# Performance work log

Measured on AMD Instinct MI355X. Metric: run time of the kernel, lower is better.

## Reference

```python
import jax, jax.numpy as jnp
import numpy as np

# Blade metric for Cl(1,3) inner product <~A B>_0: sign per basis blade =
# (-1)^{k(k-1)/2} * prod(eta_ii) with eta = diag(1,-1,-1,-1).
# Order: 1 | e0 e1 e2 e3 | e01 e02 e03 e12 e13 e23 | e012 e013 e023 e123 | e0123
BLADE_METRIC = jnp.array(
    [1.0,
     1.0, -1.0, -1.0, -1.0,
     1.0, 1.0, 1.0, -1.0, -1.0, -1.0,
     -1.0, -1.0, -1.0, 1.0,
     -1.0],
    dtype=jnp.float32,
)

B, H, N, MVC, SC = 8, 8, 1024, 8, 32


def setup_inputs() -> dict:
    key = jax.random.key(0)
    ks = jax.random.split(key, 6)
    mv_shape = (B, H, N, MVC, 16)
    s_shape = (B, H, N, SC)
    return {
        "q_mv": jax.random.normal(ks[0], mv_shape, dtype=jnp.float32),
        "k_mv": jax.random.normal(ks[1], mv_shape, dtype=jnp.float32),
        "v_mv": jax.random.normal(ks[2], mv_shape, dtype=jnp.float32),
        "q_s": jax.random.normal(ks[3], s_shape, dtype=jnp.float32),
        "k_s": jax.random.normal(ks[4], s_shape, dtype=jnp.float32),
        "v_s": jax.random.normal(ks[5], s_shape, dtype=jnp.float32),
    }


def reference(q_mv, k_mv, v_mv, q_s, k_s, v_s):
    *lead, n_out, mvc, _ = q_mv.shape
    n_in = k_mv.shape[-3]
    sc = q_s.shape[-1]
    d = 16 * mvc + sc  # total feature dim used for the softmax scale

    # Apply GA blade metric to queries, flatten mv channels, concat scalars.
    qf = jnp.concatenate(
        [(q_mv * BLADE_METRIC).reshape(*lead, n_out, mvc * 16), q_s], axis=-1
    )
    kf = jnp.concatenate([k_mv.reshape(*lead, n_in, mvc * 16), k_s], axis=-1)
    vf = jnp.concatenate([v_mv.reshape(*lead, n_in, mvc * 16), v_s], axis=-1)

    scores = jnp.einsum("bhid,bhjd->bhij", qf, kf) / jnp.sqrt(
        jnp.asarray(d, dtype=qf.dtype)
    )
    attn = jax.nn.softmax(scores, axis=-1)
    out = jnp.einsum("bhij,bhjd->bhid", attn, vf)

    out_mv = out[..., : mvc * 16].reshape(*lead, n_out, mvc, 16)
    out_s = out[..., mvc * 16 :]
    return out_mv, out_s
```

## Files before the change

### kernel.cpp

```cpp
#include <hip/hip_runtime.h>

typedef __attribute__((ext_vector_type(8))) _Float16 f16x8;
typedef __attribute__((ext_vector_type(4))) float f32x4;

#define BHn 64
#define Nn 1024

static constexpr int kOutMvElems = 8 * 8 * 1024 * 128;
static constexpr float kScaleLog2e = 0.11405506f;
static constexpr unsigned kNegMask = 0xBF1Cu;
static constexpr int kBlob = 20480;

typedef __attribute__((address_space(1))) const void* gas1_t;
typedef __attribute__((address_space(3))) void* las3_t;
__device__ __forceinline__ void dma16(const _Float16* g, _Float16* l) {
  __builtin_amdgcn_global_load_lds((gas1_t)g, (las3_t)l, 16, 0, 0);
}

__global__ __launch_bounds__(256) void pack_kernel(const float* __restrict__ kmv,
                                                   const float* __restrict__ ks,
                                                   const float* __restrict__ vmv,
                                                   const float* __restrict__ vs,
                                                   _Float16* __restrict__ KV) {
  __shared__ _Float16 tk[64][184];
  __shared__ _Float16 tv[160][72];
  const int kt = blockIdx.x;
  const int bh = blockIdx.y;
  const int tid = threadIdx.x;
#pragma unroll
  for (int i = 0; i < 5; ++i) {
    int s = tid + 256 * i;
    int key = s / 20, p = s - key * 20;
    int row = bh * Nn + kt * 64 + key;
    const float* src = (p < 16) ? (kmv + (size_t)row * 128 + p * 8)
                                : (ks + (size_t)row * 32 + (p - 16) * 8);
    float4 a = *(const float4*)src;
    float4 b = *(const float4*)(src + 4);
    f16x8 h;
    h[0] = (_Float16)a.x; h[1] = (_Float16)a.y; h[2] = (_Float16)a.z; h[3] = (_Float16)a.w;
    h[4] = (_Float16)b.x; h[5] = (_Float16)b.y; h[6] = (_Float16)b.z; h[7] = (_Float16)b.w;
    *(f16x8*)&tk[key][p * 8] = h;
  }
  for (int s = tid; s < 64 * 40; s += 256) {
    int key = s / 40, p = s - key * 40;
    int row = bh * Nn + kt * 64 + key;
    const float* src = (p < 32) ? (vmv + (size_t)row * 128 + p * 4)
                                : (vs + (size_t)row * 32 + (p - 32) * 4);
    float4 v = *(const float4*)src;
    int d = p * 4;
    tv[d + 0][key] = (_Float16)v.x;
    tv[d + 1][key] = (_Float16)v.y;
    tv[d + 2][key] = (_Float16)v.z;
    tv[d + 3][key] = (_Float16)v.w;
  }
  __syncthreads();
  _Float16* dst = KV + ((size_t)bh * 16 + kt) * kBlob;
#pragma unroll
  for (int i = 0; i < 5; ++i) {
    int u = tid + 256 * i;
    int p = u >> 6, key = u & 63;
    f16x8 h = *(const f16x8*)&tk[key][p * 8];
    *(f16x8*)&dst[p * 512 + key * 8] = h;
  }
#pragma unroll
  for (int i = 0; i < 5; ++i) {
    int u = tid + 256 * i;
    int s = u / 160, d = u - s * 160;
    int c32 = (s >> 2) * 32, gg = s & 3;
    f16x8 h;
#pragma unroll
    for (int i2 = 0; i2 < 8; ++i2) {
      int key = c32 + ((i2 < 4) ? (gg * 4 + i2) : (16 + gg * 4 + (i2 - 4)));
      h[i2] = tv[d][key];
    }
    *(f16x8*)&dst[10240 + u * 8] = h;
  }
}

__global__ __launch_bounds__(512, 2) void geo_attn_kernel(const float* __restrict__ qmv,
                                                          const float* __restrict__ qs,
                                                          const _Float16* __restrict__ KV,
                                                          float* __restrict__ out) {
  __shared__ __align__(16) _Float16 kv[2 * kBlob];

  const int b = blockIdx.x;
  const int sw = (b & 7) * 32 + (b >> 3);
  const int qb = sw & 3;
  const int bh = sw >> 2;

  const int tid = threadIdx.x;
  const int w = tid >> 6;
  const int l = tid & 63;
  const int g = l >> 4;
  const int nn = l & 15;

  const _Float16* blob0 = KV + (size_t)bh * 16 * kBlob;

  int kbase[5];
#pragma unroll
  for (int c = 0; c < 5; ++c) kbase[c] = (4 * c + g) * 512 + nn * 8;
  int vbase[2];
#pragma unroll
  for (int ch = 0; ch < 2; ++ch) vbase[ch] = 10240 + (4 * ch + g) * 1280 + nn * 8;

  f16x8 qf[2][5];
#pragma unroll
  for (int q2 = 0; q2 < 2; ++q2) {
    const size_t qbase = (size_t)(bh * Nn + qb * 256 + w * 32 + q2 * 16 + nn);
#pragma unroll
    for (int c = 0; c < 5; ++c) {
      const float* src = (c < 4) ? (qmv + qbase * 128 + c * 32 + 8 * g)
                                 : (qs + qbase * 32 + 8 * g);
      float4 a = *(const float4*)src;
      float4 bb = *(const float4*)(src + 4);
      float x[8] = {a.x, a.y, a.z, a.w, bb.x, bb.y, bb.z, bb.w};
#pragma unroll
      for (int i = 0; i < 8; ++i) {
        float v = x[i] * kScaleLog2e;
        if (c < 4) {
          int idx = ((g & 1) << 3) + i;
          v = ((kNegMask >> idx) & 1u) ? -v : v;
        }
        qf[q2][c][i] = (_Float16)v;
      }
    }
  }

  f32x4 acc[2][10];
#pragma unroll
  for (int q2 = 0; q2 < 2; ++q2)
#pragma unroll
    for (int j = 0; j < 10; ++j) acc[q2][j] = (f32x4){0.f, 0.f, 0.f, 0.f};
  float Ma = 12.f, Mb = 12.f, La = 0.f, Lb = 0.f;

  f32x4 sa[4], sb[4];
  f16x8 paf[2], pbf[2];

  const int laneOff = l * 8 + w * 512;
  auto stage = [&](int t, int buf) {
    const _Float16* src = blob0 + (size_t)t * kBlob + laneOff;
    _Float16* dst = &kv[buf * kBlob + w * 512];
#pragma unroll
    for (int i = 0; i < 5; ++i) dma16(src + i * 4096, dst + i * 4096);
  };
  auto do_qk = [&](int buf) {
    const _Float16* kb_ = &kv[buf * kBlob];
#pragma unroll
    for (int kb = 0; kb < 4; ++kb) {
      sa[kb] = (f32x4){0.f, 0.f, 0.f, 0.f};
      sb[kb] = (f32x4){0.f, 0.f, 0.f, 0.f};
    }
#pragma unroll
    for (int c = 0; c < 5; ++c) {
      f16x8 kf[4];
#pragma unroll
      for (int kb = 0; kb < 4; ++kb) kf[kb] = *(const f16x8*)&kb_[kbase[c] + kb * 128];
#pragma unroll
      for (int kb = 0; kb < 4; ++kb) {
        sa[kb] = __builtin_amdgcn_mfma_f32_16x16x32_f16(kf[kb], qf[0][c], sa[kb], 0, 0, 0);
        sb[kb] = __builtin_amdgcn_mfma_f32_16x16x32_f16(kf[kb], qf[1][c], sb[kb], 0, 0, 0);
      }
    }
  };
  auto do_pv = [&](int buf) {
    const _Float16* vb_ = &kv[buf * kBlob];
#pragma unroll
    for (int ch = 0; ch < 2; ++ch)
#pragma unroll
      for (int j = 0; j < 10; ++j) {
        f16x8 vb = *(const f16x8*)&vb_[vbase[ch] + j * 128];
        acc[0][j] = __builtin_amdgcn_mfma_f32_16x16x32_f16(paf[ch], vb, acc[0][j], 0, 0, 0);
        acc[1][j] = __builtin_amdgcn_mfma_f32_16x16x32_f16(pbf[ch], vb, acc[1][j], 0, 0, 0);
      }
  };
  auto do_softmax = [&]() {
    float lma = fmaxf(fmaxf(fmaxf(fmaxf(sa[0][0], sa[0][1]), fmaxf(sa[0][2], sa[0][3])),
                            fmaxf(fmaxf(sa[1][0], sa[1][1]), fmaxf(sa[1][2], sa[1][3]))),
                      fmaxf(fmaxf(fmaxf(sa[2][0], sa[2][1]), fmaxf(sa[2][2], sa[2][3])),
                            fmaxf(fmaxf(sa[3][0], sa[3][1]), fmaxf(sa[3][2], sa[3][3]))));
    float lmb = fmaxf(fmaxf(fmaxf(fmaxf(sb[0][0], sb[0][1]), fmaxf(sb[0][2], sb[0][3])),
                            fmaxf(fmaxf(sb[1][0], sb[1][1]), fmaxf(sb[1][2], sb[1][3]))),
                      fmaxf(fmaxf(fmaxf(sb[2][0], sb[2][1]), fmaxf(sb[2][2], sb[2][3])),
                            fmaxf(fmaxf(sb[3][0], sb[3][1]), fmaxf(sb[3][2], sb[3][3]))));
    bool need = (lma - Ma > 8.f) || (lmb - Mb > 8.f);
    if (__any((int)need)) {
      float pma = fmaxf(lma, __shfl_xor(lma, 16));
      pma = fmaxf(pma, __shfl_xor(pma, 32));
      float pmb = fmaxf(lmb, __shfl_xor(lmb, 16));
      pmb = fmaxf(pmb, __shfl_xor(pmb, 32));
      float nMa = fmaxf(Ma, pma); float fsa = exp2f(Ma - nMa); Ma = nMa;
      float nMb = fmaxf(Mb, pmb); float fsb = exp2f(Mb - nMb); Mb = nMb;
      La *= fsa; Lb *= fsb;
      float fa[4], fb[4];
#pragma unroll
      for (int r = 0; r < 4; ++r) {
        fa[r] = __shfl(fsa, 4 * g + r, 16);
        fb[r] = __shfl(fsb, 4 * g + r, 16);
      }
#pragma unroll
      for (int j = 0; j < 10; ++j)
#pragma unroll
        for (int r = 0; r < 4; ++r) {
          acc[0][j][r] *= fa[r];
          acc[1][j][r] *= fb[r];
        }
    }
    float rsa = 0.f, rsb = 0.f;
#pragma unroll
    for (int kb = 0; kb < 4; ++kb) {
      const int ch = kb >> 1, off = (kb & 1) * 4;
#pragma unroll
      for (int r = 0; r < 4; ++r) {
        float pa_ = exp2f(sa[kb][r] - Ma);
        float pb_ = exp2f(sb[kb][r] - Mb);
        rsa += pa_; rsb += pb_;
        paf[ch][off + r] = (_Float16)pa_;
        pbf[ch][off + r] = (_Float16)pb_;
      }
    }
    La += rsa;
    Lb += rsb;
  };

  stage(0, 0);
  __syncthreads();

  for (int t = 0; t < 16; ++t) {
    const int cur = t & 1;
    if (t < 15) stage(t + 1, cur ^ 1);
    __builtin_amdgcn_s_setprio(1);
    do_qk(cur);
    __builtin_amdgcn_s_setprio(0);
    do_softmax();
    __builtin_amdgcn_s_setprio(1);
    do_pv(cur);
    __builtin_amdgcn_s_setprio(0);
    __syncthreads();
  }

  La += __shfl_xor(La, 16); La += __shfl_xor(La, 32);
  Lb += __shfl_xor(Lb, 16); Lb += __shfl_xor(Lb, 32);
  float ria = 1.f / La, rib = 1.f / Lb;
  float ra[4], rb_[4];
#pragma unroll
  for (int r = 0; r < 4; ++r) {
    ra[r] = __shfl(ria, 4 * g + r, 16);
    rb_[r] = __shfl(rib, 4 * g + r, 16);
  }
  const int row0 = bh * Nn + qb * 256 + w * 32;
#pragma unroll
  for (int j = 0; j < 10; ++j) {
    const int d = 16 * j + nn;
#pragma unroll
    for (int r = 0; r < 4; ++r) {
      float v0 = acc[0][j][r] * ra[r];
      float v1 = acc[1][j][r] * rb_[r];
      const int r0 = row0 + 4 * g + r;
      const int r1 = row0 + 16 + 4 * g + r;
      if (d < 128) {
        out[(size_t)r0 * 128 + d] = v0;
        out[(size_t)r1 * 128 + d] = v1;
      } else {
        out[(size_t)kOutMvElems + (size_t)r0 * 32 + (d - 128)] = v0;
        out[(size_t)kOutMvElems + (size_t)r1 * 32 + (d - 128)] = v1;
      }
    }
  }
}

extern "C" void kernel_launch(void* const* d_in, const int* in_sizes, int n_in,
                              void* d_out, int out_size, void* d_ws, size_t ws_size,
                              hipStream_t stream) {
  const float* qmv = (const float*)d_in[0];
  const float* kmv = (const float*)d_in[1];
  const float* vmv = (const float*)d_in[2];
  const float* qs = (const float*)d_in[3];
  const float* ks = (const float*)d_in[4];
  const float* vs = (const float*)d_in[5];
  float* out = (float*)d_out;

  _Float16* KV = (_Float16*)d_ws;

  pack_kernel<<<dim3(16, BHn), dim3(256), 0, stream>>>(kmv, ks, vmv, vs, KV);
  geo_attn_kernel<<<dim3(256), dim3(512), 0, stream>>>(qmv, qs, KV, out);
}
```

Baseline: 82.61 us.

## Stage two KV blobs per barrier and defer max rescaling until sums overflow

Each pipeline stage now loads two 64-key KV blobs (double-buffered pairs in LDS), which halves the number of barriers and main-loop iterations. The online-softmax max check moves after the exponentials: probabilities are first computed against the old running max, and the max is recomputed and rescaled only when a row sum exceeds a threshold. This removes the per-tile max reduction from the common path. In exchange LDS use doubles, which can lower occupancy at two blocks per CU, and the rare overflow path recomputes the exponentials.

```diff
diff --git a/kernel.cpp b/kernel.cpp
--- a/kernel.cpp
+++ b/kernel.cpp
@@ -10,6 +10,7 @@
 static constexpr float kScaleLog2e = 0.11405506f;
 static constexpr unsigned kNegMask = 0xBF1Cu;
 static constexpr int kBlob = 20480;
+static constexpr int kPair = 2 * kBlob;
 
 typedef __attribute__((address_space(1))) const void* gas1_t;
 typedef __attribute__((address_space(3))) void* las3_t;
@@ -81,7 +82,7 @@
                                                           const float* __restrict__ qs,
                                                           const _Float16* __restrict__ KV,
                                                           float* __restrict__ out) {
-  __shared__ __align__(16) _Float16 kv[2 * kBlob];
+  __shared__ __align__(16) _Float16 kv[2 * kPair];
 
   const int b = blockIdx.x;
   const int sw = (b & 7) * 32 + (b >> 3);
@@ -138,13 +139,12 @@
 
   const int laneOff = l * 8 + w * 512;
   auto stage = [&](int t, int buf) {
-    const _Float16* src = blob0 + (size_t)t * kBlob + laneOff;
-    _Float16* dst = &kv[buf * kBlob + w * 512];
-#pragma unroll
-    for (int i = 0; i < 5; ++i) dma16(src + i * 4096, dst + i * 4096);
+    const _Float16* src = blob0 + (size_t)t * kPair + laneOff;
+    _Float16* dst = &kv[buf * kPair + laneOff];
+#pragma unroll
+    for (int i = 0; i < 10; ++i) dma16(src + i * 4096, dst + i * 4096);
   };
-  auto do_qk = [&](int buf) {
-    const _Float16* kb_ = &kv[buf * kBlob];
+  auto do_qk = [&](const _Float16* kb_) {
 #pragma unroll
     for (int kb = 0; kb < 4; ++kb) {
       sa[kb] = (f32x4){0.f, 0.f, 0.f, 0.f};
@@ -162,49 +162,17 @@
       }
     }
   };
-  auto do_pv = [&](int buf) {
-    const _Float16* vb_ = &kv[buf * kBlob];
+  auto do_pv = [&](const _Float16* vb_) {
 #pragma unroll
     for (int ch = 0; ch < 2; ++ch)
 #pragma unroll
       for (int j = 0; j < 10; ++j) {
-        f16x8 vb = *(const f16x8*)&vb_[vbase[ch] + j * 128];
+        f16x8 vb = *(const f16x8*)&vb_[vbase[ch] + j * 128 - 10240];
         acc[0][j] = __builtin_amdgcn_mfma_f32_16x16x32_f16(paf[ch], vb, acc[0][j], 0, 0, 0);
         acc[1][j] = __builtin_amdgcn_mfma_f32_16x16x32_f16(pbf[ch], vb, acc[1][j], 0, 0, 0);
       }
   };
   auto do_softmax = [&]() {
-    float lma = fmaxf(fmaxf(fmaxf(fmaxf(sa[0][0], sa[0][1]), fmaxf(sa[0][2], sa[0][3])),
-                            fmaxf(fmaxf(sa[1][0], sa[1][1]), fmaxf(sa[1][2], sa[1][3]))),
-                      fmaxf(fmaxf(fmaxf(sa[2][0], sa[2][1]), fmaxf(sa[2][2], sa[2][3])),
-                            fmaxf(fmaxf(sa[3][0], sa[3][1]), fmaxf(sa[3][2], sa[3][3]))));
-    float lmb = fmaxf(fmaxf(fmaxf(fmaxf(sb[0][0], sb[0][1]), fmaxf(sb[0][2], sb[0][3])),
-                            fmaxf(fmaxf(sb[1][0], sb[1][1]), fmaxf(sb[1][2], sb[1][3]))),
-                      fmaxf(fmaxf(fmaxf(sb[2][0], sb[2][1]), fmaxf(sb[2][2], sb[2][3])),
-                            fmaxf(fmaxf(sb[3][0], sb[3][1]), fmaxf(sb[3][2], sb[3][3]))));
-    bool need = (lma - Ma > 8.f) || (lmb - Mb > 8.f);
-    if (__any((int)need)) {
-      float pma = fmaxf(lma, __shfl_xor(lma, 16));
-      pma = fmaxf(pma, __shfl_xor(pma, 32));
-      float pmb = fmaxf(lmb, __shfl_xor(lmb, 16));
-      pmb = fmaxf(pmb, __shfl_xor(pmb, 32));
-      float nMa = fmaxf(Ma, pma); float fsa = exp2f(Ma - nMa); Ma = nMa;
-      float nMb = fmaxf(Mb, pmb); float fsb = exp2f(Mb - nMb); Mb = nMb;
-      La *= fsa; Lb *= fsb;
-      float fa[4], fb[4];
-#pragma unroll
-      for (int r = 0; r < 4; ++r) {
-        fa[r] = __shfl(fsa, 4 * g + r, 16);
-        fb[r] = __shfl(fsb, 4 * g + r, 16);
-      }
-#pragma unroll
-      for (int j = 0; j < 10; ++j)
-#pragma unroll
-        for (int r = 0; r < 4; ++r) {
-          acc[0][j][r] *= fa[r];
-          acc[1][j][r] *= fb[r];
-        }
-    }
     float rsa = 0.f, rsb = 0.f;
 #pragma unroll
     for (int kb = 0; kb < 4; ++kb) {
@@ -218,6 +186,47 @@
         pbf[ch][off + r] = (_Float16)pb_;
       }
     }
+    if (__builtin_expect(__any((int)(rsa > 3.2e4f || rsb > 3.2e4f)), 0)) {
+      float lma = sa[0][0], lmb = sb[0][0];
+#pragma unroll
+      for (int kb = 0; kb < 4; ++kb)
+#pragma unroll
+        for (int r = 0; r < 4; ++r) {
+          lma = fmaxf(lma, sa[kb][r]);
+          lmb = fmaxf(lmb, sb[kb][r]);
+        }
+      lma = fmaxf(lma, __shfl_xor(lma, 16)); lma = fmaxf(lma, __shfl_xor(lma, 32));
+      lmb = fmaxf(lmb, __shfl_xor(lmb, 16)); lmb = fmaxf(lmb, __shfl_xor(lmb, 32));
+      float nMa = fmaxf(Ma, lma); float fsa = exp2f(Ma - nMa); Ma = nMa;
+      float nMb = fmaxf(Mb, lmb); float fsb = exp2f(Mb - nMb); Mb = nMb;
+      La *= fsa; Lb *= fsb;
+      float fa[4], fb[4];
+#pragma unroll
+      for (int r = 0; r < 4; ++r) {
+        fa[r] = __shfl(fsa, 4 * g + r, 16);
+        fb[r] = __shfl(fsb, 4 * g + r, 16);
+      }
+#pragma unroll
+      for (int j = 0; j < 10; ++j)
+#pragma unroll
+        for (int r = 0; r < 4; ++r) {
+          acc[0][j][r] *= fa[r];
+          acc[1][j][r] *= fb[r];
+        }
+      rsa = 0.f; rsb = 0.f;
+#pragma unroll
+      for (int kb = 0; kb < 4; ++kb) {
+        const int ch = kb >> 1, off = (kb & 1) * 4;
+#pragma unroll
+        for (int r = 0; r < 4; ++r) {
+          float pa_ = exp2f(sa[kb][r] - Ma);
+          float pb_ = exp2f(sb[kb][r] - Mb);
+          rsa += pa_; rsb += pb_;
+          paf[ch][off + r] = (_Float16)pa_;
+          pbf[ch][off + r] = (_Float16)pb_;
+        }
+      }
+    }
     La += rsa;
     Lb += rsb;
   };
@@ -225,16 +234,21 @@
   stage(0, 0);
   __syncthreads();
 
-  for (int t = 0; t < 16; ++t) {
+  for (int t = 0; t < 8; ++t) {
     const int cur = t & 1;
-    if (t < 15) stage(t + 1, cur ^ 1);
-    __builtin_amdgcn_s_setprio(1);
-    do_qk(cur);
-    __builtin_amdgcn_s_setprio(0);
-    do_softmax();
-    __builtin_amdgcn_s_setprio(1);
-    do_pv(cur);
-    __builtin_amdgcn_s_setprio(0);
+    if (t < 7) stage(t + 1, cur ^ 1);
+    const _Float16* base = &kv[cur * kPair];
+#pragma unroll
+    for (int h = 0; h < 2; ++h) {
+      const _Float16* blob = base + h * kBlob;
+      __builtin_amdgcn_s_setprio(1);
+      do_qk(blob);
+      __builtin_amdgcn_s_setprio(0);
+      do_softmax();
+      __builtin_amdgcn_s_setprio(1);
+      do_pv(blob + 10240);
+      __builtin_amdgcn_s_setprio(0);
+    }
     __syncthreads();
   }
 
```

Result: faster. 80.86 us (-2.1%).
